# Optimization experiments

Measured on AMD Instinct MI355X. Metric: run time of the kernel, lower is better.

## Reference

```python
import jax, jax.numpy as jnp
import numpy as np

B, S, C = 1, 6, 128
Hf, Wf = 56, 100            # feature map (stride-8 of 448x800)
IMG_H, IMG_W = 448, 800
Z, Y, X = 128, 8, 128
BOUNDS = (-50.0, 50.0, -5.0, 5.0, -50.0, 50.0)
CENTROID = (0.0, 0.1, 0.0)
EPS = 1e-6


def _voxel_centers():
    # ref-frame (cam0) coordinates of voxel centers, Vox_util.Mem2Ref of gridcloud3d
    xmin, xmax = BOUNDS[0] + CENTROID[0], BOUNDS[1] + CENTROID[0]
    ymin, ymax = BOUNDS[2] + CENTROID[1], BOUNDS[3] + CENTROID[1]
    zmin, zmax = BOUNDS[4] + CENTROID[2], BOUNDS[5] + CENTROID[2]
    vsx, vsy, vsz = (xmax - xmin) / X, (ymax - ymin) / Y, (zmax - zmin) / Z
    zi, yi, xi = jnp.meshgrid(jnp.arange(Z), jnp.arange(Y), jnp.arange(X), indexing='ij')
    xr = xmin + vsx * 0.5 + xi.astype(jnp.float32) * vsx
    yr = ymin + vsy * 0.5 + yi.astype(jnp.float32) * vsy
    zr = zmin + vsz * 0.5 + zi.astype(jnp.float32) * vsz
    return jnp.stack([xr.reshape(-1), yr.reshape(-1), zr.reshape(-1)], axis=-1)  # (N,3), N=Z*Y*X


def setup_inputs() -> dict:
    key = jax.random.key(0)
    k1, k2 = jax.random.split(key)
    cam_feat = jax.random.normal(k1, (B, S, C, Hf, Wf), dtype=jnp.float32)
    # intrinsics: fx=fy=500, principal point at image center
    K = np.zeros((B, S, 4, 4), np.float32)
    K[..., 0, 0] = 500.0; K[..., 1, 1] = 500.0
    K[..., 0, 2] = IMG_W / 2.0; K[..., 1, 2] = IMG_H / 2.0
    K[..., 2, 2] = 1.0; K[..., 3, 3] = 1.0
    # surround-view rig: rotate about y (camera-frame vertical) by 2*pi*s/S
    ang = np.arange(S) * (2.0 * np.pi / S)
    c, s = np.cos(ang).astype(np.float32), np.sin(ang).astype(np.float32)
    R = np.zeros((B, S, 3, 3), np.float32)
    R[..., 0, 0] = c; R[..., 0, 2] = s; R[..., 1, 1] = 1.0
    R[..., 2, 0] = -s; R[..., 2, 2] = c
    t = np.stack([0.5 * s, np.full(S, -1.0, np.float32), 0.5 * c], axis=-1)[None].astype(np.float32)
    conv_w = jax.random.normal(k2, (C, C * Y, 3, 3), dtype=jnp.float32) * 0.02
    return {
        'cam_feat': cam_feat,
        'intrins': jnp.asarray(K),
        'rots': jnp.asarray(R),
        'trans': jnp.asarray(t),
        'conv_w': conv_w,
    }


def reference(cam_feat, intrins, rots, trans, conv_w):
    Bn, Sn = cam_feat.shape[:2]
    BS = Bn * Sn
    # velo_T_cams = [R|t]; cam0_T_camXs = inv(velo_T_cams[:,0]) @ velo_T_cams
    velo_T = (jnp.zeros((Bn, Sn, 4, 4), cam_feat.dtype)
              .at[..., :3, :3].set(rots)
              .at[..., :3, 3].set(trans)
              .at[..., 3, 3].set(1.0))
    cam0_T_camXs = jnp.einsum('bij,bsjk->bsik', jnp.linalg.inv(velo_T[:, 0]), velo_T)
    camXs_T_cam0 = jnp.linalg.inv(cam0_T_camXs)  # (B,S,4,4)
    # scale_intrinsics to feature resolution
    sx, sy = Wf / float(IMG_W), Hf / float(IMG_H)
    Kf = (jnp.zeros((Bn, Sn, 4, 4), cam_feat.dtype)
          .at[..., 0, 0].set(intrins[..., 0, 0] * sx)
          .at[..., 1, 1].set(intrins[..., 1, 1] * sy)
          .at[..., 0, 2].set(intrins[..., 0, 2] * sx)
          .at[..., 1, 2].set(intrins[..., 1, 2] * sy)
          .at[..., 2, 2].set(1.0).at[..., 3, 3].set(1.0))
    pixB_T_cam0 = jnp.einsum('bsij,bsjk->bsik', Kf, camXs_T_cam0).reshape(BS, 4, 4)
    camXs_T_cam0 = camXs_T_cam0.reshape(BS, 4, 4)

    xyz = _voxel_centers()                                   # (N,3)
    xyz1 = jnp.concatenate([xyz, jnp.ones((xyz.shape[0], 1), xyz.dtype)], axis=-1)  # (N,4)
    cam_pts = jnp.einsum('pij,nj->pni', camXs_T_cam0, xyz1)  # (BS,N,4)
    z = cam_pts[..., 2]
    pix = jnp.einsum('pij,nj->pni', pixB_T_cam0, xyz1)       # (BS,N,4)
    denom = jnp.maximum(pix[..., 2:3], EPS)
    x = pix[..., 0] / denom[..., 0]
    y = pix[..., 1] / denom[..., 0]
    valid = (x > -0.5) & (x < Wf - 0.5) & (y > -0.5) & (y < Hf - 0.5) & (z > 0.0)

    # normalize_grid2d + grid_sample(align_corners=False) unnormalization
    gx = jnp.clip(2.0 * x / (Wf - 1) - 1.0, -2.0, 2.0)
    gy = jnp.clip(2.0 * y / (Hf - 1) - 1.0, -2.0, 2.0)
    ux = ((gx + 1.0) * Wf - 1.0) * 0.5
    uy = ((gy + 1.0) * Hf - 1.0) * 0.5
    x0f, y0f = jnp.floor(ux), jnp.floor(uy)
    wx, wy = ux - x0f, uy - y0f
    x0i, y0i = x0f.astype(jnp.int32), y0f.astype(jnp.int32)

    feat = cam_feat.reshape(BS, C, Hf * Wf)

    def corner(xi, yi, w):
        inb = (xi >= 0) & (xi < Wf) & (yi >= 0) & (yi < Hf)  # zeros padding
        idx = jnp.clip(yi, 0, Hf - 1) * Wf + jnp.clip(xi, 0, Wf - 1)
        v = jnp.take_along_axis(feat, idx[:, None, :], axis=2)  # (BS,C,N)
        return v * (w * inb.astype(w.dtype))[:, None, :]

    vals = (corner(x0i, y0i, (1 - wx) * (1 - wy))
            + corner(x0i + 1, y0i, wx * (1 - wy))
            + corner(x0i, y0i + 1, (1 - wx) * wy)
            + corner(x0i + 1, y0i + 1, wx * wy))
    vals = vals * valid[:, None, :].astype(vals.dtype)
    feat_mems = vals.reshape(Bn, Sn, C, Z, Y, X)

    # reduce_masked_mean over cameras
    mask = (jnp.abs(feat_mems) > 0).astype(feat_mems.dtype)
    feat_mem = jnp.sum(feat_mems * mask, axis=1) / (EPS + jnp.sum(mask, axis=1))  # (B,C,Z,Y,X)

    # BEV compress: permute(0,1,3,2,4) -> (B, C*Y, Z, X), conv3x3 + InstanceNorm + GELU
    bev = jnp.transpose(feat_mem, (0, 1, 3, 2, 4)).reshape(Bn, C * Y, Z, X)
    out = jax.lax.conv_general_dilated(bev, conv_w, (1, 1), 'SAME',
                                       dimension_numbers=('NCHW', 'OIHW', 'NCHW'))
    mu = out.mean(axis=(2, 3), keepdims=True)
    var = out.var(axis=(2, 3), keepdims=True)
    out = (out - mu) * jax.lax.rsqrt(var + 1e-5)
    return jax.nn.gelu(out, approximate=False)
```

## Files before the change

kernel.cpp:

```cpp
#include <hip/hip_runtime.h>
#include <cmath>

#define SNUM 6
#define CNUM 128
#define HF 56
#define WF 100
#define HW (HF*WF)
#define ZN 128
#define YN 8
#define XN 128
#define NVOX (ZN*YN*XN)

typedef __attribute__((ext_vector_type(8))) short bf16x8;
typedef __attribute__((ext_vector_type(4))) float f32x4;
typedef __attribute__((ext_vector_type(4))) int   i32x4;

__device__ __forceinline__ unsigned short f2bf(float f) {
    unsigned u = __builtin_bit_cast(unsigned, f);
    unsigned r = (u + 0x7FFFu + ((u >> 16) & 1u)) >> 16;
    return (unsigned short)r;
}
__device__ __forceinline__ float bf2f(unsigned short h) {
    unsigned u = (unsigned)h << 16;
    return __builtin_bit_cast(float, u);
}

__device__ __forceinline__ void gl_lds16(const void* g, void* l) {
    __builtin_amdgcn_global_load_lds(
        (const __attribute__((address_space(1))) void*)g,
        (__attribute__((address_space(3))) void*)l, 16, 0, 0);
}
__device__ __forceinline__ void gl_lds4(const void* g, void* l) {
    __builtin_amdgcn_global_load_lds(
        (const __attribute__((address_space(1))) void*)g,
        (__attribute__((address_space(3))) void*)l, 4, 0, 0);
}

__global__ void k_setup(const float* __restrict__ intrins,
                        const float* __restrict__ rots,
                        const float* __restrict__ trans,
                        float* __restrict__ mats) {
    int s = threadIdx.x;
    if (s >= SNUM) return;
    float R0[9], Rs[9], t0[3], ts[3];
    for (int i = 0; i < 9; ++i) { R0[i] = rots[i]; Rs[i] = rots[s*9 + i]; }
    for (int i = 0; i < 3; ++i) { t0[i] = trans[i]; ts[i] = trans[s*3 + i]; }
    float M[3][4];
    float d0 = t0[0]-ts[0], d1 = t0[1]-ts[1], d2 = t0[2]-ts[2];
    for (int i = 0; i < 3; ++i) {
        for (int j = 0; j < 3; ++j)
            M[i][j] = Rs[0*3+i]*R0[0*3+j] + Rs[1*3+i]*R0[1*3+j] + Rs[2*3+i]*R0[2*3+j];
        M[i][3] = Rs[0*3+i]*d0 + Rs[1*3+i]*d1 + Rs[2*3+i]*d2;
    }
    const float sx = (float)WF/800.0f, sy = (float)HF/448.0f;
    float fx = intrins[s*16 + 0]*sx, fy = intrins[s*16 + 5]*sy;
    float cx = intrins[s*16 + 2]*sx, cy = intrins[s*16 + 6]*sy;
    float* o = mats + s*24;
    for (int j = 0; j < 4; ++j) {
        o[0*4+j]      = M[0][j];
        o[1*4+j]      = M[1][j];
        o[2*4+j]      = M[2][j];
        o[12 + 0*4+j] = fx*M[0][j] + cx*M[2][j];
        o[12 + 1*4+j] = fy*M[1][j] + cy*M[2][j];
        o[12 + 2*4+j] = M[2][j];
    }
}

__global__ __launch_bounds__(256) void k_tfeat(const float* __restrict__ cf,
                                               unsigned short* __restrict__ featT) {
    __shared__ float t[32][33];
    int s = blockIdx.z;
    int p0 = blockIdx.x * 32, c0 = blockIdx.y * 32;
    int tx = threadIdx.x, ty = threadIdx.y;
#pragma unroll
    for (int k = 0; k < 4; ++k) {
        int r = ty + k*8;
        t[r][tx] = cf[((size_t)s*CNUM + c0 + r)*HW + p0 + tx];
    }
    __syncthreads();
#pragma unroll
    for (int k = 0; k < 4; ++k) {
        int r = ty + k*8;
        featT[((size_t)s*HW + p0 + r)*CNUM + c0 + tx] = f2bf(t[tx][r]);
    }
}

__global__ __launch_bounds__(256) void k_zero(unsigned short* __restrict__ bevin2) {
    int i = blockIdx.x*256 + threadIdx.x;
    if (i >= 66048) return;
    size_t unit;
    if (i < 33280) {
        int zr = i / 16640;
        int j  = i - zr*16640;
        unit = (size_t)(zr ? 129 : 0)*16640 + j;
    } else {
        int j  = i - 33280;
        int zp = 1 + (j >> 8);
        int r  = j & 255;
        int c  = r >> 1;
        int xp = (r & 1) ? 129 : 0;
        unit = ((size_t)zp*128 + c)*130 + xp;
    }
    *(i32x4*)&bevin2[unit*8] = i32x4{0,0,0,0};
}

__global__ __launch_bounds__(256) void k_sample(const unsigned short* __restrict__ featT,
                                                const float* __restrict__ mats,
                                                unsigned short* __restrict__ bevin2) {
#pragma clang fp contract(off)
    __shared__ float xch[16][132];
    __shared__ float2 suv[16][6];
    const int tid = threadIdx.x;
    const int b = blockIdx.x;
    const int z = b >> 6, x0 = (b & 63) * 2;
    const int cl = tid & 15, vs = tid >> 4;
    const int y = vs >> 1, xs = vs & 1;
    if (tid < 96) {
        int v = tid / 6, s = tid - (tid/6)*6;
        int yi = v >> 1, xi2 = x0 + (v & 1);
        float xr = -49.609375f + (float)xi2 * 0.78125f;
        float yr = (-4.9f + 0.625f) + (float)yi * 1.25f;
        float zr = -49.609375f + (float)z * 0.78125f;
        const float* m = mats + s*24;
        float zc = m[8]*xr  + m[9]*yr  + m[10]*zr + m[11];
        float ph = m[12]*xr + m[13]*yr + m[14]*zr + m[15];
        float qh = m[16]*xr + m[17]*yr + m[18]*zr + m[19];
        float denom = fmaxf(zc, 1e-6f);
        float px = ph / denom, py = qh / denom;
        bool valid = (px > -0.5f) & (px < (float)WF - 0.5f) &
                     (py > -0.5f) & (py < (float)HF - 0.5f) & (zc > 0.0f);
        float ux = -10000.0f, uy = -10000.0f;
        if (valid) {
            float gx = 2.0f*px/((float)WF - 1.0f) - 1.0f;
            float gy = 2.0f*py/((float)HF - 1.0f) - 1.0f;
            gx = fminf(fmaxf(gx, -2.0f), 2.0f);
            gy = fminf(fmaxf(gy, -2.0f), 2.0f);
            ux = ((gx + 1.0f)*(float)WF - 1.0f)*0.5f;
            uy = ((gy + 1.0f)*(float)HF - 1.0f)*0.5f;
        }
        suv[v][s] = float2{ux, uy};
    }
    __syncthreads();

    const bf16x8 zz8 = {0,0,0,0,0,0,0,0};
    float sum[8], cnt[8];
#pragma unroll
    for (int k = 0; k < 8; ++k) { sum[k] = 0.0f; cnt[k] = 0.0f; }
    for (int s = 0; s < SNUM; ++s) {
        float2 u = suv[vs][s];
        if (u.x < -999.0f) continue;
        float x0f = floorf(u.x), y0f = floorf(u.y);
        float wx = u.x - x0f, wy = u.y - y0f;
        int ix = (int)x0f, iy = (int)y0f;
        float w00 = (1.0f-wx)*(1.0f-wy), w10 = wx*(1.0f-wy);
        float w01 = (1.0f-wx)*wy,        w11 = wx*wy;
        bool bx0 = (ix >= 0) & (ix < WF);
        bool bx1 = (ix >= -1) & (ix < WF-1);
        bool by0 = (iy >= 0) & (iy < HF);
        bool by1 = (iy >= -1) & (iy < HF-1);
        bool c00 = bx0 & by0, c10 = bx1 & by0, c01 = bx0 & by1, c11 = bx1 & by1;
        const unsigned short* fb = featT + (size_t)s * (HW*CNUM) + cl*8;
        long r0 = (long)(iy*WF + ix) * CNUM;
        bf16x8 v00 = c00 ? *(const bf16x8*)(fb + r0)                 : zz8;
        bf16x8 v10 = c10 ? *(const bf16x8*)(fb + r0 + CNUM)          : zz8;
        bf16x8 v01 = c01 ? *(const bf16x8*)(fb + r0 + WF*CNUM)       : zz8;
        bf16x8 v11 = c11 ? *(const bf16x8*)(fb + r0 + WF*CNUM + CNUM): zz8;
#pragma unroll
        for (int k = 0; k < 8; ++k) {
            float v = 0.0f;
            v = v + w00 * bf2f((unsigned short)v00[k]);
            v = v + w10 * bf2f((unsigned short)v10[k]);
            v = v + w01 * bf2f((unsigned short)v01[k]);
            v = v + w11 * bf2f((unsigned short)v11[k]);
            sum[k] += v;
            cnt[k] += (v != 0.0f) ? 1.0f : 0.0f;
        }
    }
#pragma unroll
    for (int k = 0; k < 8; ++k)
        xch[vs][cl*8 + k] = sum[k] / (1e-6f + cnt[k]);
    __syncthreads();
    {
        int c = tid >> 1, xs2 = tid & 1;
        unsigned pk[4];
#pragma unroll
        for (int j = 0; j < 4; ++j) {
            float v0 = xch[(2*j)*2 + xs2][c];
            float v1 = xch[(2*j+1)*2 + xs2][c];
            pk[j] = (unsigned)f2bf(v0) | ((unsigned)f2bf(v1) << 16);
        }
        size_t unit = ((size_t)(z+1)*128 + c)*130 + (x0 + xs2 + 1);
        *(i32x4*)&bevin2[unit*8] = i32x4{(int)pk[0], (int)pk[1], (int)pk[2], (int)pk[3]};
    }
}

__global__ __launch_bounds__(256) void k_wprep(const float* __restrict__ w,
                                               unsigned short* __restrict__ w2) {
    int i = blockIdx.x*256 + threadIdx.x;
    if (i >= 9*128*1024) return;
    int ci = i & 1023; int rest = i >> 10; int co = rest & 127; int tap = rest >> 7;
    w2[i] = f2bf(w[((size_t)co*1024 + ci)*9 + tap]);
}

__global__ __launch_bounds__(256, 2) void k_conv_mfma(
        const unsigned short* __restrict__ bevin2,
        const unsigned short* __restrict__ w2,
        float* __restrict__ out,
        float* __restrict__ psum, float* __restrict__ psq) {
    __shared__ __align__(16) unsigned short lds[2][2][12*80*8];
    const int tid  = threadIdx.x;
    const int z0   = blockIdx.x;
    const int coh  = blockIdx.y >> 1;
    const int xh   = blockIdx.y & 1;
    const int lane = tid & 63, wid = tid >> 6;
    const int wr = wid & 1, kh = wid >> 1;
    const int co_base = coh*64 + wr*32;
    const int l15 = lane & 15, lhi = lane >> 4;

    f32x4 acc[2][4];
#pragma unroll
    for (int f = 0; f < 2; ++f)
#pragma unroll
        for (int nf = 0; nf < 4; ++nf) acc[f][nf] = f32x4{0.f,0.f,0.f,0.f};

    const unsigned short* aw0 = w2 + ((size_t)(co_base      + l15))*1024 + kh*512 + lhi*8;
    const unsigned short* aw1 = w2 + ((size_t)(co_base + 16 + l15))*1024 + kh*512 + lhi*8;

    bf16x8 aC[6], aN[6];

#define STAGE(BUF, STEP)                                                       \
    {                                                                          \
        _Pragma("unroll")                                                      \
        for (int r6 = 0; r6 < 6; ++r6) {                                       \
            int r = wr*6 + r6;                                                 \
            int dzr = r >> 2, cg = r & 3;                                      \
            const unsigned short* gsrc = bevin2 +                              \
                (((size_t)(z0 + dzr)*128 + kh*64 + (STEP)*4 + cg)*130 + xh*64)*8; \
            unsigned short* ldst = &lds[kh][BUF][r*80*8];                      \
            gl_lds16(gsrc + (size_t)lane*8, ldst);                             \
            gl_lds4 (gsrc + 64*8 + (size_t)lane*2, ldst + 64*8);               \
        }                                                                      \
    }
#define A3(DST, DZ, CI0)                                                       \
    {                                                                          \
        _Pragma("unroll")                                                      \
        for (int t = 0; t < 3; ++t) {                                          \
            DST[t*2]   = *(const bf16x8*)(aw0 + (size_t)((DZ)*3+t)*131072 + (CI0)); \
            DST[t*2+1] = *(const bf16x8*)(aw1 + (size_t)((DZ)*3+t)*131072 + (CI0)); \
        }                                                                      \
    }
#define CDZ(DZ, BUF, AFR)                                                      \
    {                                                                          \
        __builtin_amdgcn_s_setprio(1);                                         \
        _Pragma("unroll")                                                      \
        for (int dx = 0; dx < 3; ++dx) {                                       \
            bf16x8 a0 = AFR[dx*2];                                             \
            bf16x8 a1 = AFR[dx*2+1];                                           \
            _Pragma("unroll")                                                  \
            for (int nf = 0; nf < 4; ++nf) {                                   \
                bf16x8 bfr = *(const bf16x8*)&lds[kh][BUF][(((DZ)*4 + lhi)*80 + nf*16 + l15 + dx)*8]; \
                acc[0][nf] = __builtin_amdgcn_mfma_f32_16x16x32_bf16(a0, bfr, acc[0][nf], 0, 0, 0); \
                acc[1][nf] = __builtin_amdgcn_mfma_f32_16x16x32_bf16(a1, bfr, acc[1][nf], 0, 0, 0); \
            }                                                                  \
        }                                                                      \
        __builtin_amdgcn_s_setprio(0);                                         \
    }

    STAGE(0, 0);
    A3(aC, 0, 0);
    __syncthreads();

    for (int ss = 0; ss < 8; ++ss) {
        const int s0 = 2*ss;
        STAGE(1, s0 + 1);
        A3(aN, 1, s0*32);        CDZ(0, 0, aC);
        A3(aC, 2, s0*32);        CDZ(1, 0, aN);
        A3(aN, 0, (s0+1)*32);    CDZ(2, 0, aC);
        __syncthreads();
        if (ss < 7) STAGE(0, s0 + 2);
        A3(aC, 1, (s0+1)*32);    CDZ(0, 1, aN);
        A3(aN, 2, (s0+1)*32);    CDZ(1, 1, aC);
        if (ss < 7) A3(aC, 0, (s0+2)*32);
        CDZ(2, 1, aN);
        if (ss < 7) __syncthreads();
    }

    __syncthreads();
    float* lds_f = (float*)&lds[0][0][0];
    if (kh == 1) {
#pragma unroll
        for (int f = 0; f < 2; ++f)
#pragma unroll
            for (int nf = 0; nf < 4; ++nf)
#pragma unroll
                for (int r = 0; r < 4; ++r)
                    lds_f[wr*2048 + (f*16 + lhi*4 + r)*64 + nf*16 + l15] = acc[f][nf][r];
    }
    __syncthreads();
    if (kh == 0) {
        float ps[2][4], pq[2][4];
#pragma unroll
        for (int f = 0; f < 2; ++f)
#pragma unroll
            for (int r = 0; r < 4; ++r) { ps[f][r] = 0.0f; pq[f][r] = 0.0f; }
#pragma unroll
        for (int f = 0; f < 2; ++f)
#pragma unroll
            for (int nf = 0; nf < 4; ++nf)
#pragma unroll
                for (int r = 0; r < 4; ++r) {
                    int co = co_base + f*16 + lhi*4 + r;
                    float v = acc[f][nf][r] + lds_f[wr*2048 + (f*16 + lhi*4 + r)*64 + nf*16 + l15];
                    out[(size_t)co*16384 + z0*128 + xh*64 + nf*16 + l15] = v;
                    ps[f][r] += v;
                    pq[f][r] += v*v;
                }
#pragma unroll
        for (int f = 0; f < 2; ++f)
#pragma unroll
            for (int r = 0; r < 4; ++r) {
                float s = ps[f][r], q = pq[f][r];
#pragma unroll
                for (int m = 1; m < 16; m <<= 1) {
                    s += __shfl_xor(s, m);
                    q += __shfl_xor(q, m);
                }
                if (l15 == 0) {
                    int co = co_base + f*16 + lhi*4 + r;
                    int pb = z0*2 + xh;
                    psum[co*256 + pb] = s;
                    psq [co*256 + pb] = q;
                }
            }
    }
#undef STAGE
#undef A3
#undef CDZ
}

__global__ __launch_bounds__(256) void k_stats(const float* __restrict__ psum,
                                               const float* __restrict__ psq,
                                               float* __restrict__ stats) {
    __shared__ float r1[256], r2[256];
    int co = blockIdx.x, tid = threadIdx.x;
    r1[tid] = psum[co*256 + tid];
    r2[tid] = psq [co*256 + tid];
    __syncthreads();
    for (int off = 128; off > 0; off >>= 1) {
        if (tid < off) { r1[tid] += r1[tid+off]; r2[tid] += r2[tid+off]; }
        __syncthreads();
    }
    if (tid == 0) {
        float mean = r1[0] * (1.0f/16384.0f);
        float var  = r2[0] * (1.0f/16384.0f) - mean*mean;
        stats[co*2]   = mean;
        stats[co*2+1] = rsqrtf(var + 1e-5f);
    }
}

__global__ __launch_bounds__(256) void k_gelu(float* __restrict__ out,
                                              const float* __restrict__ stats) {
    int i = blockIdx.x*256 + threadIdx.x;
    int co = i >> 14;
    float v = out[i];
    float r = (v - stats[co*2]) * stats[co*2+1];
    out[i] = 0.5f * r * (1.0f + erff(r * 0.70710678118654752f));
}

extern "C" void kernel_launch(void* const* d_in, const int* in_sizes, int n_in,
                              void* d_out, int out_size, void* d_ws, size_t ws_size,
                              hipStream_t stream) {
    const float* cam_feat = (const float*)d_in[0];
    const float* intrins  = (const float*)d_in[1];
    const float* rots     = (const float*)d_in[2];
    const float* trans    = (const float*)d_in[3];
    const float* conv_w   = (const float*)d_in[4];
    float* out = (float*)d_out;
    float* ws  = (float*)d_ws;

    float* mats  = ws;
    unsigned short* featT  = (unsigned short*)(ws + 160);
    unsigned short* bevin2 = featT + (size_t)SNUM*HW*CNUM;
    unsigned short* w2     = bevin2 + (size_t)130*128*130*8;
    float* psum  = (float*)(w2 + 9*128*1024);
    float* psq   = psum + 32768;
    float* stats = psq + 32768;

    hipLaunchKernelGGL(k_setup, dim3(1), dim3(64), 0, stream, intrins, rots, trans, mats);
    hipLaunchKernelGGL(k_tfeat, dim3(HW/32, CNUM/32, SNUM), dim3(32,8), 0, stream, cam_feat, featT);
    hipLaunchKernelGGL(k_wprep, dim3((9*128*1024 + 255)/256), dim3(256), 0, stream, conv_w, w2);
    hipLaunchKernelGGL(k_zero, dim3((66048 + 255)/256), dim3(256), 0, stream, bevin2);
    hipLaunchKernelGGL(k_sample, dim3(8192), dim3(256), 0, stream, featT, mats, bevin2);
    hipLaunchKernelGGL(k_conv_mfma, dim3(128, 4), dim3(256), 0, stream, bevin2, w2, out, psum, psq);
    hipLaunchKernelGGL(k_stats, dim3(128), dim3(256), 0, stream, psum, psq, stats);
    hipLaunchKernelGGL(k_gelu, dim3(8192), dim3(256), 0, stream, out, stats);
}
```

Before: 138.3 us.

## Give each conv wave all 64 output channels, halving block size to two waves

The conv kernel now runs two waves per block instead of four. Each wave computes 64 output channels (four 16-row fragments) rather than 32, so every LDS B-fragment read feeds four MFMAs instead of two. Each wave now stages all 12 LDS rows and loads twice as many weight fragments, which raises register pressure (acc 4x4 plus aC/aN of 12 each). Fewer waves per block and lower occupancy may weaken latency hiding. An unused variable in the sampling kernel is also removed.

```diff
diff --git a/kernel.cpp b/kernel.cpp
--- a/kernel.cpp
+++ b/kernel.cpp
@@ -114,7 +114,6 @@
     const int b = blockIdx.x;
     const int z = b >> 6, x0 = (b & 63) * 2;
     const int cl = tid & 15, vs = tid >> 4;
-    const int y = vs >> 1, xs = vs & 1;
     if (tid < 96) {
         int v = tid / 6, s = tid - (tid/6)*6;
         int yi = v >> 1, xi2 = x0 + (v & 1);
@@ -202,7 +201,7 @@
     w2[i] = f2bf(w[((size_t)co*1024 + ci)*9 + tap]);
 }
 
-__global__ __launch_bounds__(256, 2) void k_conv_mfma(
+__global__ __launch_bounds__(128, 1) void k_conv_mfma(
         const unsigned short* __restrict__ bevin2,
         const unsigned short* __restrict__ w2,
         float* __restrict__ out,
@@ -210,43 +209,45 @@
     __shared__ __align__(16) unsigned short lds[2][2][12*80*8];
     const int tid  = threadIdx.x;
     const int z0   = blockIdx.x;
-    const int coh  = blockIdx.y >> 1;
-    const int xh   = blockIdx.y & 1;
-    const int lane = tid & 63, wid = tid >> 6;
-    const int wr = wid & 1, kh = wid >> 1;
-    const int co_base = coh*64 + wr*32;
+    const int cob  = blockIdx.y >> 1;
+    const int xb   = blockIdx.y & 1;
+    const int lane = tid & 63, kh = tid >> 6;
+    const int co_base = cob*64;
     const int l15 = lane & 15, lhi = lane >> 4;
 
-    f32x4 acc[2][4];
-#pragma unroll
-    for (int f = 0; f < 2; ++f)
-#pragma unroll
-        for (int nf = 0; nf < 4; ++nf) acc[f][nf] = f32x4{0.f,0.f,0.f,0.f};
+    f32x4 acc[4][4];
+#pragma unroll
+    for (int cf = 0; cf < 4; ++cf)
+#pragma unroll
+        for (int nf = 0; nf < 4; ++nf) acc[cf][nf] = f32x4{0.f,0.f,0.f,0.f};
 
     const unsigned short* aw0 = w2 + ((size_t)(co_base      + l15))*1024 + kh*512 + lhi*8;
     const unsigned short* aw1 = w2 + ((size_t)(co_base + 16 + l15))*1024 + kh*512 + lhi*8;
-
-    bf16x8 aC[6], aN[6];
+    const unsigned short* aw2 = w2 + ((size_t)(co_base + 32 + l15))*1024 + kh*512 + lhi*8;
+    const unsigned short* aw3 = w2 + ((size_t)(co_base + 48 + l15))*1024 + kh*512 + lhi*8;
+
+    bf16x8 aC[12], aN[12];
 
 #define STAGE(BUF, STEP)                                                       \
     {                                                                          \
         _Pragma("unroll")                                                      \
-        for (int r6 = 0; r6 < 6; ++r6) {                                       \
-            int r = wr*6 + r6;                                                 \
+        for (int r = 0; r < 12; ++r) {                                         \
             int dzr = r >> 2, cg = r & 3;                                      \
             const unsigned short* gsrc = bevin2 +                              \
-                (((size_t)(z0 + dzr)*128 + kh*64 + (STEP)*4 + cg)*130 + xh*64)*8; \
+                (((size_t)(z0 + dzr)*128 + kh*64 + (STEP)*4 + cg)*130 + xb*64)*8; \
             unsigned short* ldst = &lds[kh][BUF][r*80*8];                      \
             gl_lds16(gsrc + (size_t)lane*8, ldst);                             \
             gl_lds4 (gsrc + 64*8 + (size_t)lane*2, ldst + 64*8);               \
         }                                                                      \
     }
-#define A3(DST, DZ, CI0)                                                       \
+#define A12(DST, DZ, CI0)                                                      \
     {                                                                          \
         _Pragma("unroll")                                                      \
         for (int t = 0; t < 3; ++t) {                                          \
-            DST[t*2]   = *(const bf16x8*)(aw0 + (size_t)((DZ)*3+t)*131072 + (CI0)); \
-            DST[t*2+1] = *(const bf16x8*)(aw1 + (size_t)((DZ)*3+t)*131072 + (CI0)); \
+            DST[t*4+0] = *(const bf16x8*)(aw0 + (size_t)((DZ)*3+t)*131072 + (CI0)); \
+            DST[t*4+1] = *(const bf16x8*)(aw1 + (size_t)((DZ)*3+t)*131072 + (CI0)); \
+            DST[t*4+2] = *(const bf16x8*)(aw2 + (size_t)((DZ)*3+t)*131072 + (CI0)); \
+            DST[t*4+3] = *(const bf16x8*)(aw3 + (size_t)((DZ)*3+t)*131072 + (CI0)); \
         }                                                                      \
     }
 #define CDZ(DZ, BUF, AFR)                                                      \
@@ -254,33 +255,33 @@
         __builtin_amdgcn_s_setprio(1);                                         \
         _Pragma("unroll")                                                      \
         for (int dx = 0; dx < 3; ++dx) {                                       \
-            bf16x8 a0 = AFR[dx*2];                                             \
-            bf16x8 a1 = AFR[dx*2+1];                                           \
             _Pragma("unroll")                                                  \
             for (int nf = 0; nf < 4; ++nf) {                                   \
                 bf16x8 bfr = *(const bf16x8*)&lds[kh][BUF][(((DZ)*4 + lhi)*80 + nf*16 + l15 + dx)*8]; \
-                acc[0][nf] = __builtin_amdgcn_mfma_f32_16x16x32_bf16(a0, bfr, acc[0][nf], 0, 0, 0); \
-                acc[1][nf] = __builtin_amdgcn_mfma_f32_16x16x32_bf16(a1, bfr, acc[1][nf], 0, 0, 0); \
+                acc[0][nf] = __builtin_amdgcn_mfma_f32_16x16x32_bf16(AFR[dx*4+0], bfr, acc[0][nf], 0, 0, 0); \
+                acc[1][nf] = __builtin_amdgcn_mfma_f32_16x16x32_bf16(AFR[dx*4+1], bfr, acc[1][nf], 0, 0, 0); \
+                acc[2][nf] = __builtin_amdgcn_mfma_f32_16x16x32_bf16(AFR[dx*4+2], bfr, acc[2][nf], 0, 0, 0); \
+                acc[3][nf] = __builtin_amdgcn_mfma_f32_16x16x32_bf16(AFR[dx*4+3], bfr, acc[3][nf], 0, 0, 0); \
             }                                                                  \
         }                                                                      \
         __builtin_amdgcn_s_setprio(0);                                         \
     }
 
     STAGE(0, 0);
-    A3(aC, 0, 0);
+    A12(aC, 0, 0);
     __syncthreads();
 
     for (int ss = 0; ss < 8; ++ss) {
         const int s0 = 2*ss;
         STAGE(1, s0 + 1);
-        A3(aN, 1, s0*32);        CDZ(0, 0, aC);
-        A3(aC, 2, s0*32);        CDZ(1, 0, aN);
-        A3(aN, 0, (s0+1)*32);    CDZ(2, 0, aC);
+        A12(aN, 1, s0*32);        CDZ(0, 0, aC);
+        A12(aC, 2, s0*32);        CDZ(1, 0, aN);
+        A12(aN, 0, (s0+1)*32);    CDZ(2, 0, aC);
         __syncthreads();
         if (ss < 7) STAGE(0, s0 + 2);
-        A3(aC, 1, (s0+1)*32);    CDZ(0, 1, aN);
-        A3(aN, 2, (s0+1)*32);    CDZ(1, 1, aC);
-        if (ss < 7) A3(aC, 0, (s0+2)*32);
+        A12(aC, 1, (s0+1)*32);    CDZ(0, 1, aN);
+        A12(aN, 2, (s0+1)*32);    CDZ(1, 1, aC);
+        if (ss < 7) A12(aC, 0, (s0+2)*32);
         CDZ(2, 1, aN);
         if (ss < 7) __syncthreads();
     }
@@ -289,52 +290,52 @@
     float* lds_f = (float*)&lds[0][0][0];
     if (kh == 1) {
 #pragma unroll
-        for (int f = 0; f < 2; ++f)
+        for (int cf = 0; cf < 4; ++cf)
 #pragma unroll
             for (int nf = 0; nf < 4; ++nf)
 #pragma unroll
                 for (int r = 0; r < 4; ++r)
-                    lds_f[wr*2048 + (f*16 + lhi*4 + r)*64 + nf*16 + l15] = acc[f][nf][r];
+                    lds_f[(cf*16 + lhi*4 + r)*64 + nf*16 + l15] = acc[cf][nf][r];
     }
     __syncthreads();
     if (kh == 0) {
-        float ps[2][4], pq[2][4];
-#pragma unroll
-        for (int f = 0; f < 2; ++f)
-#pragma unroll
-            for (int r = 0; r < 4; ++r) { ps[f][r] = 0.0f; pq[f][r] = 0.0f; }
-#pragma unroll
-        for (int f = 0; f < 2; ++f)
+        float ps[4][4], pq[4][4];
+#pragma unroll
+        for (int cf = 0; cf < 4; ++cf)
+#pragma unroll
+            for (int r = 0; r < 4; ++r) { ps[cf][r] = 0.0f; pq[cf][r] = 0.0f; }
+#pragma unroll
+        for (int cf = 0; cf < 4; ++cf)
 #pragma unroll
             for (int nf = 0; nf < 4; ++nf)
 #pragma unroll
                 for (int r = 0; r < 4; ++r) {
-                    int co = co_base + f*16 + lhi*4 + r;
-                    float v = acc[f][nf][r] + lds_f[wr*2048 + (f*16 + lhi*4 + r)*64 + nf*16 + l15];
-                    out[(size_t)co*16384 + z0*128 + xh*64 + nf*16 + l15] = v;
-                    ps[f][r] += v;
-                    pq[f][r] += v*v;
+                    int col = cf*16 + lhi*4 + r;
+                    float v = acc[cf][nf][r] + lds_f[col*64 + nf*16 + l15];
+                    out[(size_t)(co_base + col)*16384 + z0*128 + xb*64 + nf*16 + l15] = v;
+                    ps[cf][r] += v;
+                    pq[cf][r] += v*v;
                 }
 #pragma unroll
-        for (int f = 0; f < 2; ++f)
+        for (int cf = 0; cf < 4; ++cf)
 #pragma unroll
             for (int r = 0; r < 4; ++r) {
-                float s = ps[f][r], q = pq[f][r];
+                float s = ps[cf][r], q = pq[cf][r];
 #pragma unroll
                 for (int m = 1; m < 16; m <<= 1) {
                     s += __shfl_xor(s, m);
                     q += __shfl_xor(q, m);
                 }
                 if (l15 == 0) {
-                    int co = co_base + f*16 + lhi*4 + r;
-                    int pb = z0*2 + xh;
+                    int co = co_base + cf*16 + lhi*4 + r;
+                    int pb = z0*2 + xb;
                     psum[co*256 + pb] = s;
                     psq [co*256 + pb] = q;
                 }
             }
     }
 #undef STAGE
-#undef A3
+#undef A12
 #undef CDZ
 }
 
@@ -391,7 +392,7 @@
     hipLaunchKernelGGL(k_wprep, dim3((9*128*1024 + 255)/256), dim3(256), 0, stream, conv_w, w2);
     hipLaunchKernelGGL(k_zero, dim3((66048 + 255)/256), dim3(256), 0, stream, bevin2);
     hipLaunchKernelGGL(k_sample, dim3(8192), dim3(256), 0, stream, featT, mats, bevin2);
-    hipLaunchKernelGGL(k_conv_mfma, dim3(128, 4), dim3(256), 0, stream, bevin2, w2, out, psum, psq);
+    hipLaunchKernelGGL(k_conv_mfma, dim3(128, 4), dim3(128), 0, stream, bevin2, w2, out, psum, psq);
     hipLaunchKernelGGL(k_stats, dim3(128), dim3(256), 0, stream, psum, psq, stats);
     hipLaunchKernelGGL(k_gelu, dim3(8192), dim3(256), 0, stream, out, stats);
 }
```

Result: no change. 138.3 us (+0.0%).

## Restructure conv tiling: full x-row per block, drop split-K LDS reduction

Applied to the files above, without the earlier changes.

The conv kernel now gives each block a full 128-wide x row and 64 output channels, with waves split over x halves instead of over the input-channel halves. This removes the cross-wave split-K reduction through LDS at the end and lets each staged input tile be reused across both x halves. It also adds an XCD-friendly block-index swizzle and launches a 1D grid of 256 blocks. In exchange, each wave holds twice as many weight fragments in registers and the LDS tile grows, so occupancy drops to one block per SIMD set (launch bounds 256,1) and there are half as many blocks.

```diff
diff --git a/kernel.cpp b/kernel.cpp
--- a/kernel.cpp
+++ b/kernel.cpp
@@ -114,7 +114,6 @@
     const int b = blockIdx.x;
     const int z = b >> 6, x0 = (b & 63) * 2;
     const int cl = tid & 15, vs = tid >> 4;
-    const int y = vs >> 1, xs = vs & 1;
     if (tid < 96) {
         int v = tid / 6, s = tid - (tid/6)*6;
         int yi = v >> 1, xi2 = x0 + (v & 1);
@@ -202,18 +201,19 @@
     w2[i] = f2bf(w[((size_t)co*1024 + ci)*9 + tap]);
 }
 
-__global__ __launch_bounds__(256, 2) void k_conv_mfma(
+__global__ __launch_bounds__(256, 1) void k_conv_mfma(
         const unsigned short* __restrict__ bevin2,
         const unsigned short* __restrict__ w2,
         float* __restrict__ out,
         float* __restrict__ psum, float* __restrict__ psq) {
-    __shared__ __align__(16) unsigned short lds[2][2][12*80*8];
+    __shared__ __align__(16) unsigned short lds[2][24*144*8];
     const int tid  = threadIdx.x;
-    const int z0   = blockIdx.x;
-    const int coh  = blockIdx.y >> 1;
-    const int xh   = blockIdx.y & 1;
+    const int bid  = blockIdx.x;
+    const int swz  = (bid & 7)*32 + (bid >> 3);
+    const int z0   = swz & 127;
+    const int coh  = swz >> 7;
     const int lane = tid & 63, wid = tid >> 6;
-    const int wr = wid & 1, kh = wid >> 1;
+    const int wr = wid >> 1, xw = wid & 1;
     const int co_base = coh*64 + wr*32;
     const int l15 = lane & 15, lhi = lane >> 4;
 
@@ -223,118 +223,109 @@
 #pragma unroll
         for (int nf = 0; nf < 4; ++nf) acc[f][nf] = f32x4{0.f,0.f,0.f,0.f};
 
-    const unsigned short* aw0 = w2 + ((size_t)(co_base      + l15))*1024 + kh*512 + lhi*8;
-    const unsigned short* aw1 = w2 + ((size_t)(co_base + 16 + l15))*1024 + kh*512 + lhi*8;
-
-    bf16x8 aC[6], aN[6];
+    const unsigned short* aw0 = w2 + ((size_t)(co_base      + l15))*1024 + lhi*8;
+    const unsigned short* aw1 = w2 + ((size_t)(co_base + 16 + l15))*1024 + lhi*8;
+
+    bf16x8 aC[12], aN[12];
 
 #define STAGE(BUF, STEP)                                                       \
     {                                                                          \
         _Pragma("unroll")                                                      \
         for (int r6 = 0; r6 < 6; ++r6) {                                       \
-            int r = wr*6 + r6;                                                 \
-            int dzr = r >> 2, cg = r & 3;                                      \
+            int r = wid*6 + r6;                                                \
+            int zrel = r >> 3, cq = r & 7;                                     \
             const unsigned short* gsrc = bevin2 +                              \
-                (((size_t)(z0 + dzr)*128 + kh*64 + (STEP)*4 + cg)*130 + xh*64)*8; \
-            unsigned short* ldst = &lds[kh][BUF][r*80*8];                      \
+                (((size_t)(z0 + zrel)*128 + (STEP)*8 + cq)*130)*8;             \
+            unsigned short* ldst = &lds[BUF][r*144*8];                         \
             gl_lds16(gsrc + (size_t)lane*8, ldst);                             \
-            gl_lds4 (gsrc + 64*8 + (size_t)lane*2, ldst + 64*8);               \
+            gl_lds16(gsrc + (size_t)(64 + lane)*8, ldst + 64*8);               \
+            gl_lds4 (gsrc + 128*8 + (size_t)lane*2, ldst + 128*8);             \
         }                                                                      \
     }
-#define A3(DST, DZ, CI0)                                                       \
+#define A12(DST, DZ, CI0)                                                      \
     {                                                                          \
         _Pragma("unroll")                                                      \
-        for (int t = 0; t < 3; ++t) {                                          \
-            DST[t*2]   = *(const bf16x8*)(aw0 + (size_t)((DZ)*3+t)*131072 + (CI0)); \
-            DST[t*2+1] = *(const bf16x8*)(aw1 + (size_t)((DZ)*3+t)*131072 + (CI0)); \
-        }                                                                      \
+        for (int t = 0; t < 3; ++t)                                            \
+            _Pragma("unroll")                                                  \
+            for (int ks = 0; ks < 2; ++ks) {                                   \
+                DST[(t*2+ks)*2+0] = *(const bf16x8*)(aw0 + (size_t)((DZ)*3+t)*131072 + (CI0) + ks*32); \
+                DST[(t*2+ks)*2+1] = *(const bf16x8*)(aw1 + (size_t)((DZ)*3+t)*131072 + (CI0) + ks*32); \
+            }                                                                  \
     }
 #define CDZ(DZ, BUF, AFR)                                                      \
     {                                                                          \
         __builtin_amdgcn_s_setprio(1);                                         \
         _Pragma("unroll")                                                      \
-        for (int dx = 0; dx < 3; ++dx) {                                       \
-            bf16x8 a0 = AFR[dx*2];                                             \
-            bf16x8 a1 = AFR[dx*2+1];                                           \
+        for (int dx = 0; dx < 3; ++dx)                                         \
             _Pragma("unroll")                                                  \
-            for (int nf = 0; nf < 4; ++nf) {                                   \
-                bf16x8 bfr = *(const bf16x8*)&lds[kh][BUF][(((DZ)*4 + lhi)*80 + nf*16 + l15 + dx)*8]; \
-                acc[0][nf] = __builtin_amdgcn_mfma_f32_16x16x32_bf16(a0, bfr, acc[0][nf], 0, 0, 0); \
-                acc[1][nf] = __builtin_amdgcn_mfma_f32_16x16x32_bf16(a1, bfr, acc[1][nf], 0, 0, 0); \
+            for (int ks = 0; ks < 2; ++ks) {                                   \
+                bf16x8 a0 = AFR[(dx*2+ks)*2+0];                                \
+                bf16x8 a1 = AFR[(dx*2+ks)*2+1];                                \
+                _Pragma("unroll")                                              \
+                for (int nf = 0; nf < 4; ++nf) {                               \
+                    bf16x8 bfr = *(const bf16x8*)&lds[BUF][(((DZ)*8 + ks*4 + lhi)*144 + xw*64 + nf*16 + l15 + dx)*8]; \
+                    acc[0][nf] = __builtin_amdgcn_mfma_f32_16x16x32_bf16(a0, bfr, acc[0][nf], 0, 0, 0); \
+                    acc[1][nf] = __builtin_amdgcn_mfma_f32_16x16x32_bf16(a1, bfr, acc[1][nf], 0, 0, 0); \
+                }                                                              \
             }                                                                  \
-        }                                                                      \
         __builtin_amdgcn_s_setprio(0);                                         \
     }
 
     STAGE(0, 0);
-    A3(aC, 0, 0);
-    __syncthreads();
-
-    for (int ss = 0; ss < 8; ++ss) {
-        const int s0 = 2*ss;
+    A12(aC, 0, 0);
+    __syncthreads();
+
+    for (int cc = 0; cc < 8; ++cc) {
+        const int s0 = 2*cc;
         STAGE(1, s0 + 1);
-        A3(aN, 1, s0*32);        CDZ(0, 0, aC);
-        A3(aC, 2, s0*32);        CDZ(1, 0, aN);
-        A3(aN, 0, (s0+1)*32);    CDZ(2, 0, aC);
+        A12(aN, 1, s0*64);        CDZ(0, 0, aC);
+        A12(aC, 2, s0*64);        CDZ(1, 0, aN);
+        A12(aN, 0, (s0+1)*64);    CDZ(2, 0, aC);
         __syncthreads();
-        if (ss < 7) STAGE(0, s0 + 2);
-        A3(aC, 1, (s0+1)*32);    CDZ(0, 1, aN);
-        A3(aN, 2, (s0+1)*32);    CDZ(1, 1, aC);
-        if (ss < 7) A3(aC, 0, (s0+2)*32);
+        if (cc < 7) STAGE(0, s0 + 2);
+        A12(aC, 1, (s0+1)*64);    CDZ(0, 1, aN);
+        A12(aN, 2, (s0+1)*64);    CDZ(1, 1, aC);
+        if (cc < 7) A12(aC, 0, (s0+2)*64);
         CDZ(2, 1, aN);
-        if (ss < 7) __syncthreads();
-    }
-
-    __syncthreads();
-    float* lds_f = (float*)&lds[0][0][0];
-    if (kh == 1) {
-#pragma unroll
-        for (int f = 0; f < 2; ++f)
-#pragma unroll
-            for (int nf = 0; nf < 4; ++nf)
-#pragma unroll
-                for (int r = 0; r < 4; ++r)
-                    lds_f[wr*2048 + (f*16 + lhi*4 + r)*64 + nf*16 + l15] = acc[f][nf][r];
-    }
-    __syncthreads();
-    if (kh == 0) {
-        float ps[2][4], pq[2][4];
-#pragma unroll
-        for (int f = 0; f < 2; ++f)
-#pragma unroll
-            for (int r = 0; r < 4; ++r) { ps[f][r] = 0.0f; pq[f][r] = 0.0f; }
-#pragma unroll
-        for (int f = 0; f < 2; ++f)
-#pragma unroll
-            for (int nf = 0; nf < 4; ++nf)
-#pragma unroll
-                for (int r = 0; r < 4; ++r) {
-                    int co = co_base + f*16 + lhi*4 + r;
-                    float v = acc[f][nf][r] + lds_f[wr*2048 + (f*16 + lhi*4 + r)*64 + nf*16 + l15];
-                    out[(size_t)co*16384 + z0*128 + xh*64 + nf*16 + l15] = v;
-                    ps[f][r] += v;
-                    pq[f][r] += v*v;
-                }
-#pragma unroll
-        for (int f = 0; f < 2; ++f)
+        if (cc < 7) __syncthreads();
+    }
+
+    float ps[2][4], pq[2][4];
+#pragma unroll
+    for (int f = 0; f < 2; ++f)
+#pragma unroll
+        for (int r = 0; r < 4; ++r) { ps[f][r] = 0.0f; pq[f][r] = 0.0f; }
+#pragma unroll
+    for (int f = 0; f < 2; ++f)
+#pragma unroll
+        for (int nf = 0; nf < 4; ++nf)
 #pragma unroll
             for (int r = 0; r < 4; ++r) {
-                float s = ps[f][r], q = pq[f][r];
-#pragma unroll
-                for (int m = 1; m < 16; m <<= 1) {
-                    s += __shfl_xor(s, m);
-                    q += __shfl_xor(q, m);
-                }
-                if (l15 == 0) {
-                    int co = co_base + f*16 + lhi*4 + r;
-                    int pb = z0*2 + xh;
-                    psum[co*256 + pb] = s;
-                    psq [co*256 + pb] = q;
-                }
+                int co = co_base + f*16 + lhi*4 + r;
+                float v = acc[f][nf][r];
+                out[(size_t)co*16384 + z0*128 + xw*64 + nf*16 + l15] = v;
+                ps[f][r] += v;
+                pq[f][r] += v*v;
             }
-    }
+#pragma unroll
+    for (int f = 0; f < 2; ++f)
+#pragma unroll
+        for (int r = 0; r < 4; ++r) {
+            float s = ps[f][r], q = pq[f][r];
+#pragma unroll
+            for (int m = 1; m < 16; m <<= 1) {
+                s += __shfl_xor(s, m);
+                q += __shfl_xor(q, m);
+            }
+            if (l15 == 0) {
+                int co = co_base + f*16 + lhi*4 + r;
+                int pb = z0*2 + xw;
+                psum[co*256 + pb] = s;
+                psq [co*256 + pb] = q;
+            }
+        }
 #undef STAGE
-#undef A3
+#undef A12
 #undef CDZ
 }
 
@@ -391,7 +382,7 @@
     hipLaunchKernelGGL(k_wprep, dim3((9*128*1024 + 255)/256), dim3(256), 0, stream, conv_w, w2);
     hipLaunchKernelGGL(k_zero, dim3((66048 + 255)/256), dim3(256), 0, stream, bevin2);
     hipLaunchKernelGGL(k_sample, dim3(8192), dim3(256), 0, stream, featT, mats, bevin2);
-    hipLaunchKernelGGL(k_conv_mfma, dim3(128, 4), dim3(256), 0, stream, bevin2, w2, out, psum, psq);
+    hipLaunchKernelGGL(k_conv_mfma, dim3(256), dim3(256), 0, stream, bevin2, w2, out, psum, psq);
     hipLaunchKernelGGL(k_stats, dim3(128), dim3(256), 0, stream, psum, psq, stats);
     hipLaunchKernelGGL(k_gelu, dim3(8192), dim3(256), 0, stream, out, stats);
 }
```

After: 138.9 us. About the same (+0.4%).
